# Performance work log

Hardware: AMD Instinct MI355X
Metric: run time of the kernel (lower is better)

The kernel has to match this reference:

```python
import jax, jax.numpy as jnp
import numpy as np


def setup_inputs() -> dict:
    key = jax.random.key(0)
    B, L, H, D = 4, 4096, 8, 64
    sample_k = int(np.ceil(np.log(L)))  # factor=1 -> U_part = ceil(ln L_K) = 9
    k1, k2, k3, k4 = jax.random.split(key, 4)
    return {
        "queries": jax.random.normal(k1, (B, L, H, D), jnp.float32),
        "keys": jax.random.normal(k2, (B, L, H, D), jnp.float32),
        "values": jax.random.normal(k3, (B, L, H, D), jnp.float32),
        "index_sample": jax.random.randint(k4, (L, sample_k), 0, L),
    }


def _prob_attention(Q, K, V, index_sample):
    # Q, K, V: [B, H, L, D]
    B, H, L_K, D = K.shape
    L_Q = Q.shape[2]
    u = min(int(np.ceil(np.log(L_Q))), L_Q)  # n_top (static)

    # --- _prob_QK: sampled scores, sparsity measure M, top-u queries ---
    # gather sampled keys per query position: [B, H, L_Q, sample_k, D]
    K_sample = K[:, :, index_sample, :]
    QK_sample = jnp.einsum('bhld,bhlsd->bhls', Q, K_sample)  # [B,H,L_Q,S]
    M = QK_sample.max(axis=-1) - QK_sample.sum(axis=-1) / L_K  # [B,H,L_Q]
    _, M_top = jax.lax.top_k(M, u)  # [B,H,u] indices of top queries

    Q_reduce = jnp.take_along_axis(Q, M_top[..., None], axis=2)  # [B,H,u,D]
    scale = 1.0 / jnp.sqrt(jnp.asarray(D, Q.dtype))
    scores = jnp.einsum('bhud,bhkd->bhuk', Q_reduce, K) * scale  # [B,H,u,L_K]

    # --- initial context (mask_flag=False): mean of V over keys ---
    context = jnp.broadcast_to(V.mean(axis=2, keepdims=True), (B, H, L_Q, D))

    # --- update context at the top-u query positions ---
    attn = jax.nn.softmax(scores, axis=-1)  # [B,H,u,L_K]
    ctx_top = jnp.einsum('bhuk,bhkd->bhud', attn, V)  # [B,H,u,D]
    b_idx = jnp.arange(B)[:, None, None]
    h_idx = jnp.arange(H)[None, :, None]
    context = context.at[b_idx, h_idx, M_top].set(ctx_top)
    return context, attn


def reference(queries, keys, values, index_sample):
    # inputs: [B, L, H, D] -> internal [B, H, L, D]
    Q = queries.transpose(0, 2, 1, 3)
    K = keys.transpose(0, 2, 1, 3)
    V = values.transpose(0, 2, 1, 3)
    context, attn = _prob_attention(Q, K, V, index_sample)
    return context.transpose(0, 2, 1, 3), attn
```

## Files before the change

### kernel.cpp

```cpp
#include <hip/hip_runtime.h>
#include <math.h>

#define B_ 4
#define L_ 4096
#define H_ 8
#define D_ 64
#define S_ 9
#define U_ 9
#define VC_ 64
#define CC_ 16
#define TKC_ 8
#define KCH_ 32
#define NCHK_ (L_ / KCH_)
#define SCB_ (B_ * NCHK_)

#define VMBLK_ 256
#define MBLK_ 4096
#define FILLBLK_ 8192

__device__ __forceinline__ float dot4(const float4& a, const float4& b) {
    return a.x * b.x + a.y * b.y + a.z * b.z + a.w * b.w;
}

__global__ void __launch_bounds__(256, 4)
kernel_M_vmean(const float* __restrict__ Q, const float* __restrict__ K,
               const int* __restrict__ idx, float* __restrict__ M,
               const float* __restrict__ V, float* __restrict__ vpart) {
    if (blockIdx.x < VMBLK_) {
        int blk = blockIdx.x;
        int c = blk & (VC_ - 1), b = blk >> 6;
        int col = threadIdx.x & 127;
        int lp  = threadIdx.x >> 7;
        const int CHUNK = L_ / VC_;
        const float4* base = (const float4*)(V + (size_t)b * L_ * H_ * D_);
        float4 acc = make_float4(0.f, 0.f, 0.f, 0.f);
        for (int l = c * CHUNK + lp; l < (c + 1) * CHUNK; l += 2) {
            float4 v = base[(size_t)l * 128 + col];
            acc.x += v.x; acc.y += v.y; acc.z += v.z; acc.w += v.w;
        }
        __shared__ float4 red[256];
        red[threadIdx.x] = acc;
        __syncthreads();
        if (lp == 0) {
            float4 o = red[threadIdx.x + 128];
            acc.x += o.x; acc.y += o.y; acc.z += o.z; acc.w += o.w;
            ((float4*)vpart)[(size_t)blk * 128 + col] = acc;
        }
        return;
    }
    int t = threadIdx.x;
    int wid = t >> 6, lane = t & 63;
    int w = ((blockIdx.x - VMBLK_) << 2) + wid;
    int b = __builtin_amdgcn_readfirstlane(w >> 12);
    int l = __builtin_amdgcn_readfirstlane(w & (L_ - 1));

    int ki[S_];
#pragma unroll
    for (int s = 0; s < S_; ++s) ki[s] = idx[l * S_ + s];

    const float4* qb = (const float4*)(Q + (size_t)(b * L_ + l) * (H_ * D_));
    float4 q0 = qb[2 * lane];
    float4 q1 = qb[2 * lane + 1];

    const float* Kb = K + (size_t)b * L_ * (H_ * D_);

    float4 ka[S_], kc[S_];
#pragma unroll
    for (int s = 0; s < S_; ++s) {
        const float4* kp = (const float4*)(Kb + (size_t)ki[s] * (H_ * D_));
        ka[s] = kp[2 * lane];
        kc[s] = kp[2 * lane + 1];
    }

    float mx = -INFINITY, sm = 0.0f;
#pragma unroll
    for (int s = 0; s < S_; ++s) {
        float d = dot4(q0, ka[s]) + dot4(q1, kc[s]);
        d += __shfl_xor(d, 1);
        d += __shfl_xor(d, 2);
        d += __shfl_xor(d, 4);
        mx = fmaxf(mx, d);
        sm += d;
    }
    if ((lane & 7) == 0) {
        int h = lane >> 3;
        M[((size_t)(b * H_ + h) << 12) + l] = mx - sm * (1.0f / (float)L_);
    }
}

#define CSWAP(a, b)                                                          \
    if (v[b] > v[a] || (v[b] == v[a] && id[b] < id[a])) {                    \
        float tv = v[a]; v[a] = v[b]; v[b] = tv;                             \
        int ti = id[a]; id[a] = id[b]; id[b] = ti;                           \
    }

__global__ void kernel_topk1(const float* __restrict__ M,
                             float* __restrict__ cand_v, int* __restrict__ cand_i) {
    int bh = blockIdx.x >> 3;
    int chunk = blockIdx.x & (TKC_ - 1);
    int lane = threadIdx.x;
    const float* Ms = M + ((size_t)bh << 12);

    float v[8]; int id[8];
#pragma unroll
    for (int c = 0; c < 8; ++c) {
        int gi = chunk * 512 + lane + 64 * c;
        v[c] = Ms[gi]; id[c] = gi;
    }
    CSWAP(0,1) CSWAP(2,3) CSWAP(4,5) CSWAP(6,7)
    CSWAP(0,2) CSWAP(1,3) CSWAP(4,6) CSWAP(5,7)
    CSWAP(1,2) CSWAP(5,6)
    CSWAP(0,4) CSWAP(1,5) CSWAP(2,6) CSWAP(3,7)
    CSWAP(2,4) CSWAP(3,5)
    CSWAP(1,2) CSWAP(3,4) CSWAP(5,6)

    float* cv = cand_v + (size_t)blockIdx.x * U_;
    int*   ci = cand_i + (size_t)blockIdx.x * U_;
#pragma unroll
    for (int r = 0; r < U_; ++r) {
        float bv = v[0]; int bi = id[0];
#pragma unroll
        for (int off = 1; off < 64; off <<= 1) {
            float ov = __shfl_xor(bv, off);
            int   oi = __shfl_xor(bi, off);
            if (ov > bv || (ov == bv && oi < bi)) { bv = ov; bi = oi; }
        }
        if (lane == 0) { cv[r] = bv; ci[r] = bi; }
        if (id[0] == bi) {
#pragma unroll
            for (int c = 0; c < 7; ++c) { v[c] = v[c+1]; id[c] = id[c+1]; }
            v[7] = -INFINITY; id[7] = 0x7fffffff;
        }
    }
}

__global__ void kernel_small(const float* __restrict__ cand_v, const int* __restrict__ cand_i,
                             int* __restrict__ Mtop, const float* __restrict__ vpart,
                             float* __restrict__ vmean) {
    if (blockIdx.x >= 32) {
        int bh = blockIdx.x - 32;
        int h = bh & (H_ - 1), b = bh >> 3;
        int d = threadIdx.x;
        float s = 0.0f;
        for (int c = 0; c < VC_; ++c)
            s += vpart[(size_t)(b * VC_ + c) * (H_ * D_) + h * D_ + d];
        vmean[bh * D_ + d] = s * (1.0f / (float)L_);
        return;
    }
    int bh = blockIdx.x;
    int lane = threadIdx.x;
    const float* cv = cand_v + (size_t)bh * (TKC_ * U_);
    const int*   ci = cand_i + (size_t)bh * (TKC_ * U_);

    float v[2]; int id[2];
    v[0] = cv[lane]; id[0] = ci[lane];
    if (lane < TKC_ * U_ - 64) { v[1] = cv[64 + lane]; id[1] = ci[64 + lane]; }
    else { v[1] = -INFINITY; id[1] = 0x7fffffff; }
    CSWAP(0,1)

#pragma unroll
    for (int r = 0; r < U_; ++r) {
        float bv = v[0]; int bi = id[0];
#pragma unroll
        for (int off = 1; off < 64; off <<= 1) {
            float ov = __shfl_xor(bv, off);
            int   oi = __shfl_xor(bi, off);
            if (ov > bv || (ov == bv && oi < bi)) { bv = ov; bi = oi; }
        }
        if (lane == 0) Mtop[bh * U_ + r] = bi;
        if (id[0] == bi) { v[0] = v[1]; id[0] = id[1]; v[1] = -INFINITY; id[1] = 0x7fffffff; }
    }
}

__global__ void __launch_bounds__(256, 4)
kernel_fill_scores(float* __restrict__ out, const float* __restrict__ vmean,
                   const float* __restrict__ Q, const float* __restrict__ K,
                   const int* __restrict__ Mtop, float* __restrict__ raw,
                   float* __restrict__ stats) {
    if (blockIdx.x < FILLBLK_) {
        int i = blockIdx.x * 256 + threadIdx.x;
        int d4 = i & 15;
        int h  = (i >> 4) & (H_ - 1);
        int b  = i >> (4 + 3 + 12);
        ((float4*)out)[i] = ((const float4*)vmean)[(b * H_ + h) * 16 + d4];
        return;
    }
    int n = blockIdx.x - FILLBLK_;
    int b = n >> 7;
    int chunk = n & 127;
    int k0 = chunk * KCH_;

    int t = threadIdx.x;
    int w = t >> 6, lane = t & 63;
    int h = lane >> 3, dq = lane & 7;
    int bh = b * H_ + h;

    float4 q0[U_], q1[U_];
#pragma unroll
    for (int u = 0; u < U_; ++u) {
        int mi = Mtop[bh * U_ + u];
        const float4* qp = (const float4*)(Q + (size_t)((b * L_ + mi) * H_ + h) * D_);
        q0[u] = qp[2 * dq];
        q1[u] = qp[2 * dq + 1];
    }

    __shared__ float sc[H_][U_][KCH_ + 1];

    const float* Kb = K + (size_t)b * L_ * (H_ * D_);
    const float4* kp = (const float4*)(Kb + (size_t)(k0 + w * 8) * (H_ * D_));
    float4 kv0 = kp[2 * lane], kv1 = kp[2 * lane + 1];
#pragma unroll
    for (int i = 0; i < 8; ++i) {
        int kloc = w * 8 + i;
        float4 nv0, nv1;
        if (i < 7) {
            const float4* np = (const float4*)(Kb + (size_t)(k0 + kloc + 1) * (H_ * D_));
            nv0 = np[2 * lane]; nv1 = np[2 * lane + 1];
        }
        float p[U_];
#pragma unroll
        for (int u = 0; u < U_; ++u) {
            float d = dot4(q0[u], kv0) + dot4(q1[u], kv1);
            d += __shfl_xor(d, 1);
            d += __shfl_xor(d, 2);
            d += __shfl_xor(d, 4);
            p[u] = d;
        }
        float val = p[0];
#pragma unroll
        for (int u = 1; u < 8; ++u) val = (dq == u) ? p[u] : val;
        sc[h][dq][kloc] = val;
        if (dq == 0) sc[h][8][kloc] = p[8];
        kv0 = nv0; kv1 = nv1;
    }
    __syncthreads();

#pragma unroll
    for (int r = 0; r < 9; ++r) {
        int j = r * 256 + t;
        int kloc = j & 31;
        int hu = j >> 5;
        int h2 = hu / U_, u2 = hu - h2 * U_;
        raw[((size_t)(b * H_ + h2) * U_ + u2) * L_ + k0 + kloc] =
            sc[h2][u2][kloc] * 0.125f;
    }

    if (t < H_ * U_) {
        int h2 = t / U_, u2 = t - h2 * U_;
        float mxs = -INFINITY;
#pragma unroll
        for (int k = 0; k < KCH_; ++k) mxs = fmaxf(mxs, sc[h2][u2][k]);
        mxs *= 0.125f;
        float se = 0.0f;
#pragma unroll
        for (int k = 0; k < KCH_; ++k) se += expf(sc[h2][u2][k] * 0.125f - mxs);
        ((float2*)stats)[(size_t)((b * H_ + h2) * U_ + u2) * NCHK_ + chunk] =
            make_float2(mxs, se);
    }
}

__global__ void kernel_ctxf(float* __restrict__ attn, const float* __restrict__ stats,
                            const float* __restrict__ V, float* __restrict__ cpart) {
    int n = blockIdx.x;
    int x = n & 7, m = n >> 3;
    int chunk = m & (CC_ - 1);
    int bh = (m >> 4) * 8 + x;
    int h = bh & (H_ - 1), b = bh >> 3;
    int k0 = chunk * (L_ / CC_);

    int t = threadIdx.x;

    __shared__ float2 gstat[U_];
    int j = t & 31;
    for (int u = t >> 5; u < U_; u += 8) {
        const float2* srow = (const float2*)stats + (size_t)(bh * U_ + u) * NCHK_;
        float2 a = srow[j];
        float mm = a.x, ss = a.y;
#pragma unroll
        for (int c = 1; c < 4; ++c) {
            float2 b2 = srow[j + 32 * c];
            float nm = fmaxf(mm, b2.x);
            ss = ss * expf(mm - nm) + b2.y * expf(b2.x - nm);
            mm = nm;
        }
#pragma unroll
        for (int off = 1; off < 32; off <<= 1) {
            float om = __shfl_xor(mm, off, 32);
            float os = __shfl_xor(ss, off, 32);
            float nm = fmaxf(mm, om);
            ss = ss * expf(mm - nm) + os * expf(om - nm);
            mm = nm;
        }
        if (j == 0) gstat[u] = make_float2(mm, 1.0f / ss);
    }
    __syncthreads();

    __shared__ float attn_s[U_][256];
    float* arow = attn + (size_t)bh * U_ * L_ + k0;
#pragma unroll
    for (int u = 0; u < U_; ++u) {
        float xv = arow[(size_t)u * L_ + t];
        float av = expf(xv - gstat[u].x) * gstat[u].y;
        attn_s[u][t] = av;
        arow[(size_t)u * L_ + t] = av;
    }
    __syncthreads();

    int g = t >> 6, lane = t & 63;
    int kl = lane >> 4, d4 = lane & 15;

    float4 acc[U_];
#pragma unroll
    for (int u = 0; u < U_; ++u) acc[u] = make_float4(0.f, 0.f, 0.f, 0.f);

    for (int i = 0; i < 16; ++i) {
        int kloc = (g * 4 + kl) + 16 * i;
        int k = k0 + kloc;
        float4 vv = *(const float4*)(V + (size_t)((b * L_ + k) * H_ + h) * D_ + 4 * d4);
        float av[U_];
#pragma unroll
        for (int u = 0; u < U_; ++u) av[u] = attn_s[u][kloc];
#pragma unroll
        for (int u = 0; u < U_; ++u) {
            acc[u].x += av[u] * vv.x; acc[u].y += av[u] * vv.y;
            acc[u].z += av[u] * vv.z; acc[u].w += av[u] * vv.w;
        }
    }
#pragma unroll
    for (int u = 0; u < U_; ++u) {
        acc[u].x += __shfl_xor(acc[u].x, 16); acc[u].y += __shfl_xor(acc[u].y, 16);
        acc[u].z += __shfl_xor(acc[u].z, 16); acc[u].w += __shfl_xor(acc[u].w, 16);
        acc[u].x += __shfl_xor(acc[u].x, 32); acc[u].y += __shfl_xor(acc[u].y, 32);
        acc[u].z += __shfl_xor(acc[u].z, 32); acc[u].w += __shfl_xor(acc[u].w, 32);
    }
    __shared__ float4 red[U_][4][16];
    if (kl == 0) {
#pragma unroll
        for (int u = 0; u < U_; ++u) red[u][g][d4] = acc[u];
    }
    __syncthreads();
    if (t < U_ * 16) {
        int u = t >> 4, dd = t & 15;
        float4 s0 = red[u][0][dd], s1 = red[u][1][dd];
        float4 s2 = red[u][2][dd], s3 = red[u][3][dd];
        float4 s = make_float4(s0.x + s1.x + s2.x + s3.x, s0.y + s1.y + s2.y + s3.y,
                               s0.z + s1.z + s2.z + s3.z, s0.w + s1.w + s2.w + s3.w);
        ((float4*)cpart)[((size_t)(bh * CC_ + chunk) * U_ + u) * 16 + dd] = s;
    }
}

__global__ void kernel_ctx2(const float* __restrict__ cpart, const int* __restrict__ Mtop,
                            float* __restrict__ out) {
    int row = blockIdx.x;
    int u = row % U_, bh = row / U_;
    int h = bh & (H_ - 1), b = bh >> 3;
    int d = threadIdx.x;
    float s = 0.0f;
#pragma unroll
    for (int c = 0; c < CC_; ++c)
        s += cpart[((size_t)(bh * CC_ + c) * U_ + u) * 64 + d];
    int l = Mtop[bh * U_ + u];
    out[(size_t)((b * L_ + l) * H_ + h) * D_ + d] = s;
}

extern "C" void kernel_launch(void* const* d_in, const int* in_sizes, int n_in,
                              void* d_out, int out_size, void* d_ws, size_t ws_size,
                              hipStream_t stream) {
    const float* Q   = (const float*)d_in[0];
    const float* K   = (const float*)d_in[1];
    const float* V   = (const float*)d_in[2];
    const int*   idx = (const int*)d_in[3];

    float* ctx_out  = (float*)d_out;
    float* attn_out = (float*)d_out + (size_t)B_ * L_ * H_ * D_;

    float* M      = (float*)d_ws;
    float* vpart  = M + (size_t)B_ * H_ * L_;
    float* vmean  = vpart + (size_t)B_ * VC_ * H_ * D_;
    float* cpart  = vmean + B_ * H_ * D_;
    float* cand_v = cpart + (size_t)32 * CC_ * U_ * 64;
    int*   cand_i = (int*)(cand_v + 32 * TKC_ * U_);
    int*   Mtop   = cand_i + 32 * TKC_ * U_;
    float* stats  = (float*)(Mtop + 32 * U_);

    kernel_M_vmean<<<VMBLK_ + MBLK_, 256, 0, stream>>>(Q, K, idx, M, V, vpart);
    kernel_topk1<<<B_ * H_ * TKC_, 64, 0, stream>>>(M, cand_v, cand_i);
    kernel_small<<<64, 64, 0, stream>>>(cand_v, cand_i, Mtop, vpart, vmean);
    kernel_fill_scores<<<FILLBLK_ + SCB_, 256, 0, stream>>>(ctx_out, vmean, Q, K, Mtop,
                                                            attn_out, stats);
    kernel_ctxf<<<32 * CC_, 256, 0, stream>>>(attn_out, stats, V, cpart);
    kernel_ctx2<<<B_ * H_ * U_, 64, 0, stream>>>(cpart, Mtop, ctx_out);
}
```

Before: 193.3 us.

## Merge top-k stages into one kernel and fuse context reduction per head

The two-stage top-k (per-chunk candidates, then final merge) becomes a single 256-thread block per (b,h), with the candidates passed through shared memory. The vmean reduction is split across four thread groups. The attention-normalize plus attn@V kernel and the separate partial-sum reduction kernel become one 1024-thread block per (b,h) that loops over all 16 key chunks and writes the context rows directly. This removes two launches and the workspace round trip. The cost is only 32 blocks for the context stage, which leaves most CUs idle.

```diff
diff --git a/kernel.cpp b/kernel.cpp
--- a/kernel.cpp
+++ b/kernel.cpp
@@ -8,7 +8,6 @@
 #define S_ 9
 #define U_ 9
 #define VC_ 64
-#define CC_ 16
 #define TKC_ 8
 #define KCH_ 32
 #define NCHK_ (L_ / KCH_)
@@ -94,81 +93,84 @@
         int ti = id[a]; id[a] = id[b]; id[b] = ti;                           \
     }
 
-__global__ void kernel_topk1(const float* __restrict__ M,
-                             float* __restrict__ cand_v, int* __restrict__ cand_i) {
-    int bh = blockIdx.x >> 3;
-    int chunk = blockIdx.x & (TKC_ - 1);
-    int lane = threadIdx.x;
-    const float* Ms = M + ((size_t)bh << 12);
-
-    float v[8]; int id[8];
-#pragma unroll
-    for (int c = 0; c < 8; ++c) {
-        int gi = chunk * 512 + lane + 64 * c;
-        v[c] = Ms[gi]; id[c] = gi;
-    }
-    CSWAP(0,1) CSWAP(2,3) CSWAP(4,5) CSWAP(6,7)
-    CSWAP(0,2) CSWAP(1,3) CSWAP(4,6) CSWAP(5,7)
-    CSWAP(1,2) CSWAP(5,6)
-    CSWAP(0,4) CSWAP(1,5) CSWAP(2,6) CSWAP(3,7)
-    CSWAP(2,4) CSWAP(3,5)
-    CSWAP(1,2) CSWAP(3,4) CSWAP(5,6)
-
-    float* cv = cand_v + (size_t)blockIdx.x * U_;
-    int*   ci = cand_i + (size_t)blockIdx.x * U_;
-#pragma unroll
-    for (int r = 0; r < U_; ++r) {
-        float bv = v[0]; int bi = id[0];
-#pragma unroll
-        for (int off = 1; off < 64; off <<= 1) {
-            float ov = __shfl_xor(bv, off);
-            int   oi = __shfl_xor(bi, off);
-            if (ov > bv || (ov == bv && oi < bi)) { bv = ov; bi = oi; }
-        }
-        if (lane == 0) { cv[r] = bv; ci[r] = bi; }
-        if (id[0] == bi) {
-#pragma unroll
-            for (int c = 0; c < 7; ++c) { v[c] = v[c+1]; id[c] = id[c+1]; }
-            v[7] = -INFINITY; id[7] = 0x7fffffff;
-        }
-    }
-}
-
-__global__ void kernel_small(const float* __restrict__ cand_v, const int* __restrict__ cand_i,
-                             int* __restrict__ Mtop, const float* __restrict__ vpart,
-                             float* __restrict__ vmean) {
+__global__ void kernel_topk(const float* __restrict__ M, int* __restrict__ Mtop,
+                            const float* __restrict__ vpart, float* __restrict__ vmean) {
+    int t = threadIdx.x;
     if (blockIdx.x >= 32) {
         int bh = blockIdx.x - 32;
         int h = bh & (H_ - 1), b = bh >> 3;
-        int d = threadIdx.x;
+        int d = t & 63, q = t >> 6;
         float s = 0.0f;
-        for (int c = 0; c < VC_; ++c)
+        for (int c = q; c < VC_; c += 4)
             s += vpart[(size_t)(b * VC_ + c) * (H_ * D_) + h * D_ + d];
-        vmean[bh * D_ + d] = s * (1.0f / (float)L_);
+        __shared__ float vr[4][64];
+        vr[q][d] = s;
+        __syncthreads();
+        if (t < 64)
+            vmean[bh * D_ + t] = (vr[0][t] + vr[1][t] + vr[2][t] + vr[3][t])
+                                 * (1.0f / (float)L_);
         return;
     }
     int bh = blockIdx.x;
-    int lane = threadIdx.x;
-    const float* cv = cand_v + (size_t)bh * (TKC_ * U_);
-    const int*   ci = cand_i + (size_t)bh * (TKC_ * U_);
-
-    float v[2]; int id[2];
-    v[0] = cv[lane]; id[0] = ci[lane];
-    if (lane < TKC_ * U_ - 64) { v[1] = cv[64 + lane]; id[1] = ci[64 + lane]; }
-    else { v[1] = -INFINITY; id[1] = 0x7fffffff; }
-    CSWAP(0,1)
-
-#pragma unroll
-    for (int r = 0; r < U_; ++r) {
-        float bv = v[0]; int bi = id[0];
-#pragma unroll
-        for (int off = 1; off < 64; off <<= 1) {
-            float ov = __shfl_xor(bv, off);
-            int   oi = __shfl_xor(bi, off);
-            if (ov > bv || (ov == bv && oi < bi)) { bv = ov; bi = oi; }
-        }
-        if (lane == 0) Mtop[bh * U_ + r] = bi;
-        if (id[0] == bi) { v[0] = v[1]; id[0] = id[1]; v[1] = -INFINITY; id[1] = 0x7fffffff; }
+    int w = t >> 6, lane = t & 63;
+    const float* Ms = M + ((size_t)bh << 12);
+
+    __shared__ float cvl[TKC_ * U_];
+    __shared__ int   cil[TKC_ * U_];
+
+#pragma unroll
+    for (int pass = 0; pass < 2; ++pass) {
+        int chunk = w * 2 + pass;
+        float v[8]; int id[8];
+#pragma unroll
+        for (int c = 0; c < 8; ++c) {
+            int gi = chunk * 512 + lane + 64 * c;
+            v[c] = Ms[gi]; id[c] = gi;
+        }
+        CSWAP(0,1) CSWAP(2,3) CSWAP(4,5) CSWAP(6,7)
+        CSWAP(0,2) CSWAP(1,3) CSWAP(4,6) CSWAP(5,7)
+        CSWAP(1,2) CSWAP(5,6)
+        CSWAP(0,4) CSWAP(1,5) CSWAP(2,6) CSWAP(3,7)
+        CSWAP(2,4) CSWAP(3,5)
+        CSWAP(1,2) CSWAP(3,4) CSWAP(5,6)
+#pragma unroll
+        for (int r = 0; r < U_; ++r) {
+            float bv = v[0]; int bi = id[0];
+#pragma unroll
+            for (int off = 1; off < 64; off <<= 1) {
+                float ov = __shfl_xor(bv, off);
+                int   oi = __shfl_xor(bi, off);
+                if (ov > bv || (ov == bv && oi < bi)) { bv = ov; bi = oi; }
+            }
+            if (lane == 0) { cvl[chunk * U_ + r] = bv; cil[chunk * U_ + r] = bi; }
+            if (id[0] == bi) {
+#pragma unroll
+                for (int c = 0; c < 7; ++c) { v[c] = v[c+1]; id[c] = id[c+1]; }
+                v[7] = -INFINITY; id[7] = 0x7fffffff;
+            }
+        }
+    }
+    __syncthreads();
+
+    if (w == 0) {
+        float v[2]; int id[2];
+        v[0] = cvl[lane]; id[0] = cil[lane];
+        if (lane < TKC_ * U_ - 64) { v[1] = cvl[64 + lane]; id[1] = cil[64 + lane]; }
+        else { v[1] = -INFINITY; id[1] = 0x7fffffff; }
+        CSWAP(0,1)
+#pragma unroll
+        for (int r = 0; r < U_; ++r) {
+            float bv = v[0]; int bi = id[0];
+#pragma unroll
+            for (int off = 1; off < 64; off <<= 1) {
+                float ov = __shfl_xor(bv, off);
+                int   oi = __shfl_xor(bi, off);
+                if (ov > bv || (ov == bv && oi < bi)) { bv = ov; bi = oi; }
+            }
+            if (lane == 0) Mtop[bh * U_ + r] = bi;
+            if (id[0] == bi) { v[0] = v[1]; id[0] = id[1];
+                               v[1] = -INFINITY; id[1] = 0x7fffffff; }
+        }
     }
 }
 
@@ -259,73 +261,84 @@
     }
 }
 
-__global__ void kernel_ctxf(float* __restrict__ attn, const float* __restrict__ stats,
-                            const float* __restrict__ V, float* __restrict__ cpart) {
-    int n = blockIdx.x;
-    int x = n & 7, m = n >> 3;
-    int chunk = m & (CC_ - 1);
-    int bh = (m >> 4) * 8 + x;
+__global__ void __launch_bounds__(1024, 1)
+kernel_ctxf2(float* __restrict__ attn, const float* __restrict__ stats,
+             const float* __restrict__ V, const int* __restrict__ Mtop,
+             float* __restrict__ out) {
+    int bh = blockIdx.x;
     int h = bh & (H_ - 1), b = bh >> 3;
-    int k0 = chunk * (L_ / CC_);
-
     int t = threadIdx.x;
-
-    __shared__ float2 gstat[U_];
-    int j = t & 31;
-    for (int u = t >> 5; u < U_; u += 8) {
-        const float2* srow = (const float2*)stats + (size_t)(bh * U_ + u) * NCHK_;
-        float2 a = srow[j];
-        float mm = a.x, ss = a.y;
-#pragma unroll
-        for (int c = 1; c < 4; ++c) {
-            float2 b2 = srow[j + 32 * c];
-            float nm = fmaxf(mm, b2.x);
-            ss = ss * expf(mm - nm) + b2.y * expf(b2.x - nm);
-            mm = nm;
-        }
-#pragma unroll
-        for (int off = 1; off < 32; off <<= 1) {
-            float om = __shfl_xor(mm, off, 32);
-            float os = __shfl_xor(ss, off, 32);
-            float nm = fmaxf(mm, om);
-            ss = ss * expf(mm - nm) + os * expf(om - nm);
-            mm = nm;
-        }
-        if (j == 0) gstat[u] = make_float2(mm, 1.0f / ss);
-    }
-    __syncthreads();
-
-    __shared__ float attn_s[U_][256];
-    float* arow = attn + (size_t)bh * U_ * L_ + k0;
-#pragma unroll
-    for (int u = 0; u < U_; ++u) {
-        float xv = arow[(size_t)u * L_ + t];
-        float av = expf(xv - gstat[u].x) * gstat[u].y;
-        attn_s[u][t] = av;
-        arow[(size_t)u * L_ + t] = av;
-    }
-    __syncthreads();
-
     int g = t >> 6, lane = t & 63;
     int kl = lane >> 4, d4 = lane & 15;
 
+    __shared__ float2 gstat[U_];
+    __shared__ float attn_s[U_][256];
+    __shared__ float4 redc[U_][16][16];
+
+    {
+        int u = t >> 5, j = t & 31;
+        if (u < U_) {
+            const float2* srow = (const float2*)stats + (size_t)(bh * U_ + u) * NCHK_;
+            float2 a = srow[j];
+            float mm = a.x, ss = a.y;
+#pragma unroll
+            for (int c = 1; c < 4; ++c) {
+                float2 b2 = srow[j + 32 * c];
+                float nm = fmaxf(mm, b2.x);
+                ss = ss * expf(mm - nm) + b2.y * expf(b2.x - nm);
+                mm = nm;
+            }
+#pragma unroll
+            for (int off = 1; off < 32; off <<= 1) {
+                float om = __shfl_xor(mm, off, 32);
+                float os = __shfl_xor(ss, off, 32);
+                float nm = fmaxf(mm, om);
+                ss = ss * expf(mm - nm) + os * expf(om - nm);
+                mm = nm;
+            }
+            if (j == 0) gstat[u] = make_float2(mm, 1.0f / ss);
+        }
+    }
+    __syncthreads();
+
     float4 acc[U_];
 #pragma unroll
     for (int u = 0; u < U_; ++u) acc[u] = make_float4(0.f, 0.f, 0.f, 0.f);
 
-    for (int i = 0; i < 16; ++i) {
-        int kloc = (g * 4 + kl) + 16 * i;
-        int k = k0 + kloc;
-        float4 vv = *(const float4*)(V + (size_t)((b * L_ + k) * H_ + h) * D_ + 4 * d4);
-        float av[U_];
-#pragma unroll
-        for (int u = 0; u < U_; ++u) av[u] = attn_s[u][kloc];
-#pragma unroll
-        for (int u = 0; u < U_; ++u) {
-            acc[u].x += av[u] * vv.x; acc[u].y += av[u] * vv.y;
-            acc[u].z += av[u] * vv.z; acc[u].w += av[u] * vv.w;
-        }
-    }
+    float* arow = attn + (size_t)bh * U_ * L_;
+
+    for (int c = 0; c < 16; ++c) {
+        int k0 = c * 256;
+#pragma unroll
+        for (int r = 0; r < 3; ++r) {
+            int idx = r * 1024 + t;
+            if (idx < U_ * 256) {
+                int u = idx >> 8, kk = idx & 255;
+                float xv = arow[(size_t)u * L_ + k0 + kk];
+                float av = expf(xv - gstat[u].x) * gstat[u].y;
+                attn_s[u][kk] = av;
+                arow[(size_t)u * L_ + k0 + kk] = av;
+            }
+        }
+        __syncthreads();
+
+#pragma unroll
+        for (int i = 0; i < 4; ++i) {
+            int kloc = (g * 4 + kl) + 64 * i;
+            int k = k0 + kloc;
+            float4 vv = *(const float4*)(V + (size_t)((b * L_ + k) * H_ + h) * D_ + 4 * d4);
+            float av[U_];
+#pragma unroll
+            for (int u = 0; u < U_; ++u) av[u] = attn_s[u][kloc];
+#pragma unroll
+            for (int u = 0; u < U_; ++u) {
+                acc[u].x += av[u] * vv.x; acc[u].y += av[u] * vv.y;
+                acc[u].z += av[u] * vv.z; acc[u].w += av[u] * vv.w;
+            }
+        }
+        __syncthreads();
+    }
+
 #pragma unroll
     for (int u = 0; u < U_; ++u) {
         acc[u].x += __shfl_xor(acc[u].x, 16); acc[u].y += __shfl_xor(acc[u].y, 16);
@@ -333,34 +346,23 @@
         acc[u].x += __shfl_xor(acc[u].x, 32); acc[u].y += __shfl_xor(acc[u].y, 32);
         acc[u].z += __shfl_xor(acc[u].z, 32); acc[u].w += __shfl_xor(acc[u].w, 32);
     }
-    __shared__ float4 red[U_][4][16];
     if (kl == 0) {
 #pragma unroll
-        for (int u = 0; u < U_; ++u) red[u][g][d4] = acc[u];
+        for (int u = 0; u < U_; ++u) redc[u][g][d4] = acc[u];
     }
     __syncthreads();
+
     if (t < U_ * 16) {
         int u = t >> 4, dd = t & 15;
-        float4 s0 = red[u][0][dd], s1 = red[u][1][dd];
-        float4 s2 = red[u][2][dd], s3 = red[u][3][dd];
-        float4 s = make_float4(s0.x + s1.x + s2.x + s3.x, s0.y + s1.y + s2.y + s3.y,
-                               s0.z + s1.z + s2.z + s3.z, s0.w + s1.w + s2.w + s3.w);
-        ((float4*)cpart)[((size_t)(bh * CC_ + chunk) * U_ + u) * 16 + dd] = s;
-    }
-}
-
-__global__ void kernel_ctx2(const float* __restrict__ cpart, const int* __restrict__ Mtop,
-                            float* __restrict__ out) {
-    int row = blockIdx.x;
-    int u = row % U_, bh = row / U_;
-    int h = bh & (H_ - 1), b = bh >> 3;
-    int d = threadIdx.x;
-    float s = 0.0f;
-#pragma unroll
-    for (int c = 0; c < CC_; ++c)
-        s += cpart[((size_t)(bh * CC_ + c) * U_ + u) * 64 + d];
-    int l = Mtop[bh * U_ + u];
-    out[(size_t)((b * L_ + l) * H_ + h) * D_ + d] = s;
+        float4 s = make_float4(0.f, 0.f, 0.f, 0.f);
+#pragma unroll
+        for (int gg = 0; gg < 16; ++gg) {
+            float4 p = redc[u][gg][dd];
+            s.x += p.x; s.y += p.y; s.z += p.z; s.w += p.w;
+        }
+        int l = Mtop[bh * U_ + u];
+        ((float4*)(out + (size_t)((b * L_ + l) * H_ + h) * D_))[dd] = s;
+    }
 }
 
 extern "C" void kernel_launch(void* const* d_in, const int* in_sizes, int n_in,
@@ -377,17 +379,12 @@
     float* M      = (float*)d_ws;
     float* vpart  = M + (size_t)B_ * H_ * L_;
     float* vmean  = vpart + (size_t)B_ * VC_ * H_ * D_;
-    float* cpart  = vmean + B_ * H_ * D_;
-    float* cand_v = cpart + (size_t)32 * CC_ * U_ * 64;
-    int*   cand_i = (int*)(cand_v + 32 * TKC_ * U_);
-    int*   Mtop   = cand_i + 32 * TKC_ * U_;
+    int*   Mtop   = (int*)(vmean + B_ * H_ * D_);
     float* stats  = (float*)(Mtop + 32 * U_);
 
     kernel_M_vmean<<<VMBLK_ + MBLK_, 256, 0, stream>>>(Q, K, idx, M, V, vpart);
-    kernel_topk1<<<B_ * H_ * TKC_, 64, 0, stream>>>(M, cand_v, cand_i);
-    kernel_small<<<64, 64, 0, stream>>>(cand_v, cand_i, Mtop, vpart, vmean);
+    kernel_topk<<<64, 256, 0, stream>>>(M, Mtop, vpart, vmean);
     kernel_fill_scores<<<FILLBLK_ + SCB_, 256, 0, stream>>>(ctx_out, vmean, Q, K, Mtop,
                                                             attn_out, stats);
-    kernel_ctxf<<<32 * CC_, 256, 0, stream>>>(attn_out, stats, V, cpart);
-    kernel_ctx2<<<B_ * H_ * U_, 64, 0, stream>>>(cpart, Mtop, ctx_out);
-}
+    kernel_ctxf2<<<32, 1024, 0, stream>>>(attn_out, stats, V, Mtop, ctx_out);
+}
```

Measured after the change: 221.3 us. 1.14x slower.
